# Optimization experiments

Measured on AMD Instinct MI355X. Metric: run time of the kernel, lower is better.

Reference implementation:

```python
import jax, jax.numpy as jnp
import numpy as np

# Central first difference with zero (same) padding along `axis`:
# out[i] = f[i+1] - f[i-1], zeros outside the domain (conv3d w/ [-1,0,1] kernel, same pad).
def d1(f, axis):
    pad = [(0, 0)] * f.ndim
    pad[axis] = (1, 1)
    fp = jnp.pad(f, pad)
    hi = tuple(slice(2, None) if a == axis else slice(None) for a in range(f.ndim))
    lo = tuple(slice(None, -2) if a == axis else slice(None) for a in range(f.ndim))
    return fp[hi] - fp[lo]

# Second difference: f[i+1] - 2 f[i] + f[i-1], zero padded.
def d2(f, axis):
    pad = [(0, 0)] * f.ndim
    pad[axis] = (1, 1)
    fp = jnp.pad(f, pad)
    hi = tuple(slice(2, None) if a == axis else slice(None) for a in range(f.ndim))
    lo = tuple(slice(None, -2) if a == axis else slice(None) for a in range(f.ndim))
    return fp[hi] - 2.0 * f + fp[lo]

AX_T, AX_X, AX_Y = 2, 3, 4  # [B, C, T, X, Y]
D_t = lambda f: d1(f, AX_T)
D_x = lambda f: d1(f, AX_X)
D_y = lambda f: d1(f, AX_Y)
D_xx_yy = lambda f: d2(f, AX_X) + d2(f, AX_Y)  # Laplacian in x,y


def setup_inputs() -> dict:
    key = jax.random.key(0)
    B, C, T, X, Y = 8, 4, 64, 128, 128
    vars_ = jax.random.normal(key, (B, C, T, X, Y), dtype=jnp.float32)
    return {
        "vars": vars_,
        "dx": jnp.float32(0.0078),
        "dt": jnp.float32(0.05),
        "eta": jnp.float32(0.01),
        "zeta": jnp.float32(0.01),
    }


def reference(vars, dx, dt, eta, zeta):
    rho = vars[:, 0:1]
    u = vars[:, 1:2]
    v = vars[:, 2:3]
    p = vars[:, 3:4]

    # mass residual (final, rescaled assignment in the torch source;
    # `self.rho` there is the continuity-eq density field rho)
    mass = (D_t(rho) * dx
            + rho * (D_x(u) + D_y(v)) * dt
            + u * D_x(rho) * dt
            + v * D_y(rho) * dt)

    div = D_x(u) + D_y(v)
    bulk = zeta + eta / 3.0

    mom_x = (rho * D_t(u) * 2.0 * dx ** 2
             + u * D_x(u) * 2.0 * dt * dx
             + v * D_y(u) * 2.0 * dt * dx
             + D_x(p) * 2.0 * dt * dx
             - eta * D_xx_yy(u) * 4.0 * dt
             - bulk * D_x(div) * 2.0 * dt)
    mom_y = (rho * D_t(v) * 2.0 * dx ** 2
             + u * D_x(v) * 2.0 * dt * dx
             + v * D_y(v) * 2.0 * dt * dx
             + D_y(p) * 2.0 * dt * dx
             - eta * D_xx_yy(v) * 4.0 * dt
             - bulk * D_y(div) * 2.0 * dt)
    mom = mom_x + mom_y

    # boundary=False path: strip 1-cell boundary in t, x, y; stack residuals on channel
    inner = (Ellipsis, slice(1, -1), slice(1, -1), slice(1, -1))
    return jnp.concatenate([mass[inner], mom[inner]], axis=1)
```

## Files before the change

### kernel.cpp

```cpp
#include <hip/hip_runtime.h>


typedef float vf4 __attribute__((ext_vector_type(4)));
typedef float vf4u __attribute__((ext_vector_type(4), aligned(4)));

__device__ __forceinline__ vf4 ld4(const float* __restrict__ p) {
    return *reinterpret_cast<const vf4u*>(p);
}

#define SH(lo, hi, s) __builtin_shufflevector(lo, hi, 2 + (s), 3 + (s), 4 + (s), 5 + (s))

__global__ __launch_bounds__(256) void cns_residuals_kernel(
    const float* __restrict__ vars,
    const float* __restrict__ s_dx, const float* __restrict__ s_dt,
    const float* __restrict__ s_eta, const float* __restrict__ s_zeta,
    float* __restrict__ out)
{
    const float dx = s_dx[0], dt = s_dt[0], eta = s_eta[0], zeta = s_zeta[0];
    const float bulk = zeta + eta * (1.0f / 3.0f);
    const float c1 = 2.0f * dx * dx;
    const float c2 = 2.0f * dt * dx;
    const float c3 = 4.0f * dt;
    const float c4 = 2.0f * dt;

    const int tid = blockIdx.x * 256 + threadIdx.x;
    const int j = tid & 31;
    int r = tid >> 5;
    const int xp = r % 126; r /= 126;
    const int tp = r % 62;  const int b = r / 62;
    const int x = xp + 1, t = tp + 1;
    const int yb = 1 + 4 * j;

    const size_t plane = 16384;
    const size_t cstr  = (size_t)64 * plane;

    const float* base = vars + (size_t)b * 4 * cstr + (size_t)t * plane
                      + ((size_t)x << 7) + yb;
    const float* R0 = base;
    const float* U0 = base + cstr;
    const float* V0 = base + 2 * cstr;
    const float* P0 = base + 3 * cstr;

    const float mLo = (j == 0)  ? 0.0f : 1.0f;
    const float mHi = (j == 31) ? 0.0f : 1.0f;

#define WIN(ptr, off, lo, hi) \
    vf4 lo = ld4((ptr) + (off) - 2); vf4 hi = ld4((ptr) + (off) + 2); \
    lo[0] *= mLo; hi[1] *= mHi; hi[2] *= mHi; hi[3] *= mHi;

    WIN(R0, 0,    r0lo, r0hi)
    WIN(U0, 0,    u0lo, u0hi)
    WIN(U0, 128,  uplo, uphi)
    WIN(U0, -128, umlo, umhi)
    WIN(V0, 0,    v0lo, v0hi)
    WIN(V0, 128,  vplo, vphi)
    WIN(V0, -128, vmlo, vmhi)
    WIN(P0, 0,    p0lo, p0hi)
#undef WIN

    const vf4 rxp = ld4(R0 + 128), rxm = ld4(R0 - 128);
    const vf4 rtp = ld4(R0 + plane), rtm = ld4(R0 - plane);
    const vf4 utp = ld4(U0 + plane), utm = ld4(U0 - plane);
    const vf4 vtp = ld4(V0 + plane), vtm = ld4(V0 - plane);
    const vf4 pxp = ld4(P0 + 128), pxm = ld4(P0 - 128);
    const vf4 zero = {0.0f, 0.0f, 0.0f, 0.0f};
    const vf4 uxp2 = (x <= 125) ? ld4(U0 + 256) : zero;
    const vf4 uxm2 = (x >= 2)   ? ld4(U0 - 256) : zero;

    const vf4 rho = SH(r0lo, r0hi, 0);
    const vf4 u   = SH(u0lo, u0hi, 0);
    const vf4 v   = SH(v0lo, v0hi, 0);

    const vf4 uxp = SH(uplo, uphi, 0), uxm = SH(umlo, umhi, 0);
    const vf4 uyp = SH(u0lo, u0hi, 1), uym = SH(u0lo, u0hi, -1);
    const vf4 vxp = SH(vplo, vphi, 0), vxm = SH(vmlo, vmhi, 0);
    const vf4 vyp = SH(v0lo, v0hi, 1), vym = SH(v0lo, v0hi, -1);

    const vf4 Dt_rho = rtp - rtm;
    const vf4 Dx_rho = rxp - rxm;
    const vf4 Dy_rho = SH(r0lo, r0hi, 1) - SH(r0lo, r0hi, -1);
    const vf4 Dx_u = uxp - uxm, Dy_u = uyp - uym;
    const vf4 Dx_v = vxp - vxm, Dy_v = vyp - vym;

    const vf4 mass = Dt_rho * dx + rho * (Dx_u + Dy_v) * dt
                   + u * Dx_rho * dt + v * Dy_rho * dt;

    const vf4 Dt_u = utp - utm, Dt_v = vtp - vtm;
    const vf4 Dx_p = pxp - pxm;
    const vf4 Dy_p = SH(p0lo, p0hi, 1) - SH(p0lo, p0hi, -1);
    const vf4 lap_u = uxp + uxm + uyp + uym - 4.0f * u;
    const vf4 lap_v = vxp + vxm + vyp + vym - 4.0f * v;

    const vf4 Dx_div = uxp2 - 2.0f * u + uxm2
                     + SH(vplo, vphi, 1) - SH(vplo, vphi, -1)
                     - SH(vmlo, vmhi, 1) + SH(vmlo, vmhi, -1);
    const vf4 Dy_div = SH(v0lo, v0hi, 2) - 2.0f * v + SH(v0lo, v0hi, -2)
                     + SH(uplo, uphi, 1) - SH(umlo, umhi, 1)
                     - SH(uplo, uphi, -1) + SH(umlo, umhi, -1);

    const vf4 mom = rho * (Dt_u + Dt_v) * c1
                  + (u * Dx_u + v * Dy_u + u * Dx_v + v * Dy_v) * c2
                  + (Dx_p + Dy_p) * c2
                  - eta * (lap_u + lap_v) * c3
                  - bulk * (Dx_div + Dy_div) * c4;

    const size_t oplane = 126 * 126;
    const size_t ocstr  = (size_t)62 * oplane;
    float* o1 = out + (size_t)b * 2 * ocstr + (size_t)tp * oplane
              + (size_t)xp * 126 + 4 * j;
    float* o2 = o1 + ocstr;
    if (j < 31) {
        *reinterpret_cast<vf4u*>(o1) = mass;
        *reinterpret_cast<vf4u*>(o2) = mom;
    } else {
        o1[0] = mass[0]; o1[1] = mass[1];
        o2[0] = mom[0];  o2[1] = mom[1];
    }
}

extern "C" void kernel_launch(void* const* d_in, const int* in_sizes, int n_in,
                              void* d_out, int out_size, void* d_ws, size_t ws_size,
                              hipStream_t stream) {
    const float* vars   = (const float*)d_in[0];
    const float* s_dx   = (const float*)d_in[1];
    const float* s_dt   = (const float*)d_in[2];
    const float* s_eta  = (const float*)d_in[3];
    const float* s_zeta = (const float*)d_in[4];
    float* out = (float*)d_out;

    const int grid = 7812;
    hipLaunchKernelGGL(cns_residuals_kernel, dim3(grid), dim3(256), 0, stream,
                       vars, s_dx, s_dt, s_eta, s_zeta, out);
}
```

Before: 44.68 us.

## Use 64-lane wave per row with 2 outputs per lane and shuffle-based y-halos

Remaps work so a full 64-wide wavefront covers one x-row with two outputs per lane, replacing overlapping float4 window loads with a single aligned float2 load plus cross-lane shuffles for the y neighbours. It also swizzles block indices across 8 groups, presumably to spread them over XCDs or improve locality, and switches output writes to nontemporal stores. The grid doubles to match. This cuts redundant global loads but adds shuffle instructions and more threads, and it relies on wave64 shuffle semantics at the row edges.

```diff
diff --git a/kernel.cpp b/kernel.cpp
--- a/kernel.cpp
+++ b/kernel.cpp
@@ -1,14 +1,37 @@
 #include <hip/hip_runtime.h>
 
 
-typedef float vf4 __attribute__((ext_vector_type(4)));
-typedef float vf4u __attribute__((ext_vector_type(4), aligned(4)));
+typedef float vf2 __attribute__((ext_vector_type(2)));
+typedef float vf2u __attribute__((ext_vector_type(2), aligned(4)));
 
-__device__ __forceinline__ vf4 ld4(const float* __restrict__ p) {
-    return *reinterpret_cast<const vf4u*>(p);
+__device__ __forceinline__ vf2 ld2(const float* p) {
+    return *reinterpret_cast<const vf2u*>(p);
 }
 
-#define SH(lo, hi, s) __builtin_shufflevector(lo, hi, 2 + (s), 3 + (s), 4 + (s), 5 + (s))
+struct W3 { vf2 c, p, m; };
+__device__ __forceinline__ W3 win(vf2 v) {
+    const float d0 = __shfl_down(v.x, 1);
+    const float d1 = __shfl_down(v.y, 1);
+    W3 w;
+    w.c = (vf2){v.y, d0};
+    w.p = (vf2){d0, d1};
+    w.m = v;
+    return w;
+}
+struct W5 { vf2 c, p, m, p2, m2; };
+__device__ __forceinline__ W5 win5(vf2 v, float mLo, float mD2) {
+    const float um = __shfl_up(v.y, 1) * mLo;
+    const float d0 = __shfl_down(v.x, 1);
+    const float d1 = __shfl_down(v.y, 1);
+    const float d2 = __shfl_down(v.x, 2) * mD2;
+    W5 w;
+    w.c  = (vf2){v.y, d0};
+    w.p  = (vf2){d0, d1};
+    w.m  = v;
+    w.p2 = (vf2){d1, d2};
+    w.m2 = (vf2){um, v.x};
+    return w;
+}
 
 __global__ __launch_bounds__(256) void cns_residuals_kernel(
     const float* __restrict__ vars,
@@ -23,83 +46,79 @@
     const float c3 = 4.0f * dt;
     const float c4 = 2.0f * dt;
 
-    const int tid = blockIdx.x * 256 + threadIdx.x;
-    const int j = tid & 31;
-    int r = tid >> 5;
+    const int i = blockIdx.x;
+    const int lb = (i & 7) * 1953 + (i >> 3);
+
+    const int tid = lb * 256 + threadIdx.x;
+    const int j = tid & 63;
+    int r = tid >> 6;
     const int xp = r % 126; r /= 126;
     const int tp = r % 62;  const int b = r / 62;
     const int x = xp + 1, t = tp + 1;
-    const int yb = 1 + 4 * j;
+    const int q = 2 * j;
 
     const size_t plane = 16384;
     const size_t cstr  = (size_t)64 * plane;
 
-    const float* base = vars + (size_t)b * 4 * cstr + (size_t)t * plane
-                      + ((size_t)x << 7) + yb;
-    const float* R0 = base;
-    const float* U0 = base + cstr;
-    const float* V0 = base + 2 * cstr;
-    const float* P0 = base + 3 * cstr;
+    const float* baseA = vars + (size_t)b * 4 * cstr + (size_t)t * plane
+                       + ((size_t)x << 7) + q;
+    const float* Rrow = baseA;
+    const float* Urow = baseA + cstr;
+    const float* Vrow = baseA + 2 * cstr;
+    const float* Prow = baseA + 3 * cstr;
 
     const float mLo = (j == 0)  ? 0.0f : 1.0f;
-    const float mHi = (j == 31) ? 0.0f : 1.0f;
+    const float mD2 = (j >= 62) ? 0.0f : 1.0f;
 
-#define WIN(ptr, off, lo, hi) \
-    vf4 lo = ld4((ptr) + (off) - 2); vf4 hi = ld4((ptr) + (off) + 2); \
-    lo[0] *= mLo; hi[1] *= mHi; hi[2] *= mHi; hi[3] *= mHi;
+    const W3 Rw  = win(ld2(Rrow));
+    const W3 Uwm = win(ld2(Urow - 128));
+    const W3 Uw0 = win(ld2(Urow));
+    const W3 Uw1 = win(ld2(Urow + 128));
+    const W3 Vwm = win(ld2(Vrow - 128));
+    const W5 Vw0 = win5(ld2(Vrow), mLo, mD2);
+    const W3 Vw1 = win(ld2(Vrow + 128));
+    const W3 Pw  = win(ld2(Prow));
 
-    WIN(R0, 0,    r0lo, r0hi)
-    WIN(U0, 0,    u0lo, u0hi)
-    WIN(U0, 128,  uplo, uphi)
-    WIN(U0, -128, umlo, umhi)
-    WIN(V0, 0,    v0lo, v0hi)
-    WIN(V0, 128,  vplo, vphi)
-    WIN(V0, -128, vmlo, vmhi)
-    WIN(P0, 0,    p0lo, p0hi)
-#undef WIN
+    const vf2 rxp = ld2(Rrow + 129),  rxm = ld2(Rrow - 127);
+    const vf2 pxp = ld2(Prow + 129),  pxm = ld2(Prow - 127);
+    const vf2 rtp = ld2(Rrow + plane + 1), rtm = ld2(Rrow - plane + 1);
+    const vf2 utp = ld2(Urow + plane + 1), utm = ld2(Urow - plane + 1);
+    const vf2 vtp = ld2(Vrow + plane + 1), vtm = ld2(Vrow - plane + 1);
+    const vf2 zero = {0.0f, 0.0f};
+    const vf2 uxp2 = (x <= 125) ? ld2(Urow + 257) : zero;
+    const vf2 uxm2 = (x >= 2)   ? ld2(Urow - 255) : zero;
 
-    const vf4 rxp = ld4(R0 + 128), rxm = ld4(R0 - 128);
-    const vf4 rtp = ld4(R0 + plane), rtm = ld4(R0 - plane);
-    const vf4 utp = ld4(U0 + plane), utm = ld4(U0 - plane);
-    const vf4 vtp = ld4(V0 + plane), vtm = ld4(V0 - plane);
-    const vf4 pxp = ld4(P0 + 128), pxm = ld4(P0 - 128);
-    const vf4 zero = {0.0f, 0.0f, 0.0f, 0.0f};
-    const vf4 uxp2 = (x <= 125) ? ld4(U0 + 256) : zero;
-    const vf4 uxm2 = (x >= 2)   ? ld4(U0 - 256) : zero;
+    const vf2 rho = Rw.c;
+    const vf2 u   = Uw0.c;
+    const vf2 v   = Vw0.c;
 
-    const vf4 rho = SH(r0lo, r0hi, 0);
-    const vf4 u   = SH(u0lo, u0hi, 0);
-    const vf4 v   = SH(v0lo, v0hi, 0);
+    const vf2 uxp = Uw1.c, uxm = Uwm.c;
+    const vf2 uyp = Uw0.p, uym = Uw0.m;
+    const vf2 vxp = Vw1.c, vxm = Vwm.c;
+    const vf2 vyp = Vw0.p, vym = Vw0.m;
 
-    const vf4 uxp = SH(uplo, uphi, 0), uxm = SH(umlo, umhi, 0);
-    const vf4 uyp = SH(u0lo, u0hi, 1), uym = SH(u0lo, u0hi, -1);
-    const vf4 vxp = SH(vplo, vphi, 0), vxm = SH(vmlo, vmhi, 0);
-    const vf4 vyp = SH(v0lo, v0hi, 1), vym = SH(v0lo, v0hi, -1);
+    const vf2 Dt_rho = rtp - rtm;
+    const vf2 Dx_rho = rxp - rxm;
+    const vf2 Dy_rho = Rw.p - Rw.m;
+    const vf2 Dx_u = uxp - uxm, Dy_u = uyp - uym;
+    const vf2 Dx_v = vxp - vxm, Dy_v = vyp - vym;
 
-    const vf4 Dt_rho = rtp - rtm;
-    const vf4 Dx_rho = rxp - rxm;
-    const vf4 Dy_rho = SH(r0lo, r0hi, 1) - SH(r0lo, r0hi, -1);
-    const vf4 Dx_u = uxp - uxm, Dy_u = uyp - uym;
-    const vf4 Dx_v = vxp - vxm, Dy_v = vyp - vym;
-
-    const vf4 mass = Dt_rho * dx + rho * (Dx_u + Dy_v) * dt
+    const vf2 mass = Dt_rho * dx + rho * (Dx_u + Dy_v) * dt
                    + u * Dx_rho * dt + v * Dy_rho * dt;
 
-    const vf4 Dt_u = utp - utm, Dt_v = vtp - vtm;
-    const vf4 Dx_p = pxp - pxm;
-    const vf4 Dy_p = SH(p0lo, p0hi, 1) - SH(p0lo, p0hi, -1);
-    const vf4 lap_u = uxp + uxm + uyp + uym - 4.0f * u;
-    const vf4 lap_v = vxp + vxm + vyp + vym - 4.0f * v;
+    const vf2 Dt_u = utp - utm, Dt_v = vtp - vtm;
+    const vf2 Dx_p = pxp - pxm;
+    const vf2 Dy_p = Pw.p - Pw.m;
+    const vf2 lap_u = uxp + uxm + uyp + uym - 4.0f * u;
+    const vf2 lap_v = vxp + vxm + vyp + vym - 4.0f * v;
 
-    const vf4 Dx_div = uxp2 - 2.0f * u + uxm2
-                     + SH(vplo, vphi, 1) - SH(vplo, vphi, -1)
-                     - SH(vmlo, vmhi, 1) + SH(vmlo, vmhi, -1);
-    const vf4 Dy_div = SH(v0lo, v0hi, 2) - 2.0f * v + SH(v0lo, v0hi, -2)
-                     + SH(uplo, uphi, 1) - SH(umlo, umhi, 1)
-                     - SH(uplo, uphi, -1) + SH(umlo, umhi, -1);
+    const vf2 Dx_div = uxp2 - 2.0f * u + uxm2
+                     + Vw1.p - Vw1.m - Vwm.p + Vwm.m;
+    const vf2 Dy_div = Vw0.p2 - 2.0f * v + Vw0.m2
+                     + Uw1.p - Uwm.p - Uw1.m + Uwm.m;
 
-    const vf4 mom = rho * (Dt_u + Dt_v) * c1
-                  + (u * Dx_u + v * Dy_u + u * Dx_v + v * Dy_v) * c2
+    const vf2 mom = rho * (Dt_u + Dt_v) * c1
+                  + (u * (Dx_u + Dx_v) + v * (Dy_u + Dy_v)) * c2
                   + (Dx_p + Dy_p) * c2
                   - eta * (lap_u + lap_v) * c3
                   - bulk * (Dx_div + Dy_div) * c4;
@@ -107,14 +126,11 @@
     const size_t oplane = 126 * 126;
     const size_t ocstr  = (size_t)62 * oplane;
     float* o1 = out + (size_t)b * 2 * ocstr + (size_t)tp * oplane
-              + (size_t)xp * 126 + 4 * j;
+              + (size_t)xp * 126 + q;
     float* o2 = o1 + ocstr;
-    if (j < 31) {
-        *reinterpret_cast<vf4u*>(o1) = mass;
-        *reinterpret_cast<vf4u*>(o2) = mom;
-    } else {
-        o1[0] = mass[0]; o1[1] = mass[1];
-        o2[0] = mom[0];  o2[1] = mom[1];
+    if (j < 63) {
+        __builtin_nontemporal_store(mass, reinterpret_cast<vf2u*>(o1));
+        __builtin_nontemporal_store(mom,  reinterpret_cast<vf2u*>(o2));
     }
 }
 
@@ -128,7 +144,7 @@
     const float* s_zeta = (const float*)d_in[4];
     float* out = (float*)d_out;
 
-    const int grid = 7812;
+    const int grid = 15624;
     hipLaunchKernelGGL(cns_residuals_kernel, dim3(grid), dim3(256), 0, stream,
                        vars, s_dx, s_dt, s_eta, s_zeta, out);
 }
```

Result: slower. 47.18 us (+5.6%).
